# Performance work log

Hardware: AMD Instinct MI355X
Metric: run time of the kernel (lower is better)

The kernel has to match this reference:

```python
import jax, jax.numpy as jnp
import numpy as np

T_EPS = 1e-07
NUM_CAPSULE = 10
DIM_CAPSULE = 64
ROUTINGS = 5


def squash(x, axis=-1):
    # NOTE: this repo's 'squash' is just norm-division (no s/(1+s) factor)
    s = jnp.sum(x * x, axis=axis, keepdims=True)
    return x / jnp.sqrt(s + T_EPS)


def setup_inputs() -> dict:
    key = jax.random.key(0)
    k1, k2 = jax.random.split(key)
    B, N, D = 128, 512, 300
    M = NUM_CAPSULE * DIM_CAPSULE  # 640
    x = jax.random.normal(k1, (B, N, D), dtype=jnp.float32)
    # xavier_normal for shape (1, D, M): std = sqrt(2/(fan_in+fan_out))
    std = float(np.sqrt(2.0 / (D + M)))
    W = jax.random.normal(k2, (1, D, M), dtype=jnp.float32) * std
    return {"x": x, "W": W}


def reference(x, W):
    B, N, D = x.shape
    # u_hat_vecs: [B, num_capsule(i), input_num_capsule(j), dim_capsule(k)]
    u = jnp.einsum('bnd,dm->bnm', x, W[0])
    u = u.reshape(B, N, NUM_CAPSULE, DIM_CAPSULE).transpose(0, 2, 1, 3)
    b = jnp.zeros((B, NUM_CAPSULE, N), dtype=x.dtype)
    outputs = None
    for i in range(ROUTINGS):
        # softmax over the num_capsule axis (axis=1 of b), matching the
        # permute(0,2,1) -> softmax(dim=2) -> permute back in torch
        c = jax.nn.softmax(b, axis=1)
        outputs = squash(jnp.einsum('bij,bijk->bik', c, u))  # [B, num, dim]
        if i < ROUTINGS - 1:
            b = jnp.einsum('bik,bijk->bij', outputs, u)
    return outputs
```

## Files before the change

### kernel.cpp

```cpp
#include <hip/hip_runtime.h>
#include <hip/hip_bf16.h>
#include <stdint.h>

#define BQ 128
#define NJ 512
#define DD 300
#define NC 10
#define DC 64
#define MM 640
#define KP 320
#define RT 5

typedef __attribute__((ext_vector_type(8))) short short8;
typedef __attribute__((ext_vector_type(4))) float f32x4;


__global__ void k_cast_x(const float* __restrict__ x, __hip_bfloat16* __restrict__ xb) {
    int g = blockIdx.x * 256 + threadIdx.x;
    int row = g / 40, cg2 = g - row * 40;
    const float* src = x + (size_t)row * DD + cg2 * 8;
    float4 a = make_float4(0.f, 0.f, 0.f, 0.f), b4 = a;
    if (cg2 < 37) { a = *(const float4*)src; b4 = *(const float4*)(src + 4); }
    else if (cg2 == 37) { a = *(const float4*)src; }
    union { ushort u[8]; uint4 v; } o;
    float f[8] = {a.x, a.y, a.z, a.w, b4.x, b4.y, b4.z, b4.w};
#pragma unroll
    for (int e = 0; e < 8; ++e) {
        __hip_bfloat16 hh = __float2bfloat16(f[e]);
        o.u[e] = *(ushort*)&hh;
    }
    *(uint4*)(xb + (size_t)row * KP + cg2 * 8) = o.v;
}

__global__ void k_cast_w(const float* __restrict__ w, __hip_bfloat16* __restrict__ wt) {
    int idx = blockIdx.x * 256 + threadIdx.x;
    int m = idx / KP, k = idx - m * KP;
    float v = (k < DD) ? w[(size_t)k * MM + m] : 0.f;
    wt[idx] = __float2bfloat16(v);
}

__global__ void k_zero(float4* __restrict__ p) {
    p[blockIdx.x * 256 + threadIdx.x] = make_float4(0.f, 0.f, 0.f, 0.f);
}


__global__ __launch_bounds__(256)
void k_gemm(const __hip_bfloat16* __restrict__ A,
            const __hip_bfloat16* __restrict__ Bt,
            __hip_bfloat16* __restrict__ C,
            float* __restrict__ su) {
    __shared__ __align__(16) __hip_bfloat16 As[128 * 64];
    __shared__ __align__(16) __hip_bfloat16 Bs[128 * 64];

    const int L  = blockIdx.x;
    const int n0 = ((L >> 3) % 5) * 128;
    const int m0 = ((L / 40) * 8 + (L & 7)) * 128;
    const int t  = threadIdx.x;
    const int w  = t >> 6, lane = t & 63;
    const int wrow = (w >> 1) * 64, wcol = (w & 1) * 64;
    const int quad = lane >> 4, r = lane & 15;

    f32x4 acc[4][4] = {};

    const int srow = t >> 3;
    const int sl   = (t & 7) ^ (srow & 7);
    const __hip_bfloat16* ag = A  + (size_t)(m0 + srow) * KP + sl * 8;
    const __hip_bfloat16* bg = Bt + (size_t)(n0 + srow) * KP + sl * 8;

    for (int kt = 0; kt < KP / 64; ++kt) {
        __syncthreads();
#pragma unroll
        for (int s = 0; s < 4; ++s) {
            __builtin_amdgcn_global_load_lds(
                (const __attribute__((address_space(1))) void*)(ag + (size_t)s * 32 * KP + kt * 64),
                (__attribute__((address_space(3))) void*)(&As[s * 2048 + t * 8]), 16, 0, 0);
            __builtin_amdgcn_global_load_lds(
                (const __attribute__((address_space(1))) void*)(bg + (size_t)s * 32 * KP + kt * 64),
                (__attribute__((address_space(3))) void*)(&Bs[s * 2048 + t * 8]), 16, 0, 0);
        }
        __syncthreads();

#pragma unroll
        for (int hh = 0; hh < 2; ++hh) {
            short8 af[4], bf[4];
#pragma unroll
            for (int mi = 0; mi < 4; ++mi) {
                int rho = wrow + mi * 16 + r;
                int p = (hh * 4 + quad) ^ (rho & 7);
                af[mi] = *(const short8*)&As[rho * 64 + p * 8];
            }
#pragma unroll
            for (int ni = 0; ni < 4; ++ni) {
                int rho = wcol + ni * 16 + r;
                int p = (hh * 4 + quad) ^ (rho & 7);
                bf[ni] = *(const short8*)&Bs[rho * 64 + p * 8];
            }
#pragma unroll
            for (int mi = 0; mi < 4; ++mi)
#pragma unroll
                for (int ni = 0; ni < 4; ++ni)
                    acc[mi][ni] = __builtin_amdgcn_mfma_f32_16x16x32_bf16(
                        af[mi], bf[ni], acc[mi][ni], 0, 0, 0);
        }
    }

#pragma unroll
    for (int mi = 0; mi < 4; ++mi)
#pragma unroll
        for (int ni = 0; ni < 4; ++ni) {
            int col = n0 + wcol + ni * 16 + r;
#pragma unroll
            for (int p = 0; p < 4; ++p) {
                int row = m0 + wrow + mi * 16 + quad * 4 + p;
                C[(size_t)row * MM + col] = __float2bfloat16(acc[mi][ni][p]);
            }
        }

    float cs[4];
#pragma unroll
    for (int ni = 0; ni < 4; ++ni) {
        float s = 0.f;
#pragma unroll
        for (int mi = 0; mi < 4; ++mi)
#pragma unroll
            for (int p = 0; p < 4; ++p) s += acc[mi][ni][p];
        s += __shfl_xor(s, 16, 64);
        s += __shfl_xor(s, 32, 64);
        cs[ni] = s;
    }
    if (quad == 0) {
        int bb = m0 >> 9;
#pragma unroll
        for (int ni = 0; ni < 4; ++ni)
            atomicAdd(&su[(size_t)bb * MM + n0 + wcol + ni * 16 + r], cs[ni]);
    }
}


#define TJ 16
#define NT 8
#define TILE_BYTES (TJ * MM * 2)

__global__ __launch_bounds__(512)
void k_pass(const __hip_bfloat16* __restrict__ u, const float* __restrict__ pprev,
            float* __restrict__ pnext, int first) {
    __shared__ __align__(16) char smem[TILE_BYTES + 32 * 161 * 4 + 160 * 4 + MM * 4];
    ushort* ub    = (ushort*)smem;
    float*  red   = (float*)(smem + TILE_BYTES);
    float*  blj   = (float*)(smem + TILE_BYTES + 20608);
    float*  outl  = (float*)(smem + TILE_BYTES + 20608 + 640);
    float*  pored = (float*)smem;

    const int t   = threadIdx.x;
    const int blk = blockIdx.x;
    const int b   = blk >> 2, q = blk & 3;
    const int w   = t >> 6, lane = t & 63;
    const int jd  = t >> 5, kg = t & 31;

    const char* ubase = (const char*)(u + (size_t)(b * NJ + q * 128) * MM);

    uint4 sa = *(const uint4*)(ubase + t * 16);
    uint4 sb = *(const uint4*)(ubase + 8192 + t * 16);
    uint2 sc = *(const uint2*)(ubase + 16384 + t * 8);

    if (w < 5) {
        float s0, s1;
        if (first) {
            s0 = 0.1f * pprev[(size_t)b * MM + w * 64 + lane];
            s1 = 0.1f * pprev[(size_t)b * MM + 320 + w * 64 + lane];
        } else {
            const float* pp = pprev + (size_t)b * 4 * MM;
            s0 = 0.f; s1 = 0.f;
#pragma unroll
            for (int qq = 0; qq < 4; ++qq) {
                s0 += pp[qq * MM + w * 64 + lane];
                s1 += pp[qq * MM + 320 + w * 64 + lane];
            }
        }
        float q0 = s0 * s0, q1 = s1 * s1;
#pragma unroll
        for (int m = 32; m >= 1; m >>= 1) {
            q0 += __shfl_xor(q0, m, 64);
            q1 += __shfl_xor(q1, m, 64);
        }
        outl[w * 64 + lane]       = s0 * rsqrtf(q0 + 1e-7f);
        outl[320 + w * 64 + lane] = s1 * rsqrtf(q1 + 1e-7f);
    }

    float po[20];
#pragma unroll
    for (int e = 0; e < 20; ++e) po[e] = 0.f;

    for (int tt = 0; tt < NT; ++tt) {
        uint4 na, nb; uint2 nc2;
        if (tt + 1 < NT) {
            const char* ns = ubase + (size_t)(tt + 1) * TILE_BYTES;
            na  = *(const uint4*)(ns + t * 16);
            nb  = *(const uint4*)(ns + 8192 + t * 16);
            nc2 = *(const uint2*)(ns + 16384 + t * 8);
        }
        __syncthreads();
        *(uint4*)((char*)ub + t * 16)        = sa;
        *(uint4*)((char*)ub + 8192 + t * 16) = sb;
        *(uint2*)((char*)ub + 16384 + t * 8) = sc;
        __syncthreads();

        const ushort* urow = ub + jd * MM;
        uint uv[10];
#pragma unroll
        for (int i = 0; i < 10; ++i)
            uv[i] = *(const uint*)(urow + i * 64 + kg * 2);

#pragma unroll
        for (int i = 0; i < 10; ++i) {
            float u0 = __uint_as_float(uv[i] << 16);
            float u1 = __uint_as_float(uv[i] & 0xffff0000u);
            float2 oo = *(const float2*)(outl + i * 64 + kg * 2);
            red[kg * 161 + jd * 10 + i] = u0 * oo.x + u1 * oo.y;
        }
        __syncthreads();
        if (t < 160) {
            float s = 0.f;
#pragma unroll
            for (int g = 0; g < 32; ++g) s += red[g * 161 + t];
            blj[t] = s;
        }
        __syncthreads();
        float c[10];
        {
            float bl[10], mx = -1e30f;
#pragma unroll
            for (int i = 0; i < 10; ++i) { bl[i] = blj[jd * 10 + i]; mx = fmaxf(mx, bl[i]); }
            float ssum = 0.f;
#pragma unroll
            for (int i = 0; i < 10; ++i) { bl[i] = __expf(bl[i] - mx); ssum += bl[i]; }
            float inv = 1.f / ssum;
#pragma unroll
            for (int i = 0; i < 10; ++i) c[i] = bl[i] * inv;
        }
#pragma unroll
        for (int i = 0; i < 10; ++i) {
            float u0 = __uint_as_float(uv[i] << 16);
            float u1 = __uint_as_float(uv[i] & 0xffff0000u);
            po[i * 2 + 0] += c[i] * u0;
            po[i * 2 + 1] += c[i] * u1;
        }
        sa = na; sb = nb; sc = nc2;
    }

#pragma unroll
    for (int e = 0; e < 20; ++e) po[e] += __shfl_xor(po[e], 32, 64);
    __syncthreads();
    if ((t & 63) < 32) {
#pragma unroll
        for (int e = 0; e < 20; ++e) pored[(w * 32 + kg) * 20 + e] = po[e];
    }
    __syncthreads();
    for (int m = t; m < MM; m += 512) {
        int i = m >> 6, k = m & 63, kg2 = k >> 1, kd = k & 1;
        float s = 0.f;
#pragma unroll
        for (int ww = 0; ww < 8; ++ww) s += pored[(ww * 32 + kg2) * 20 + i * 2 + kd];
        pnext[(size_t)blk * MM + m] = s;
    }
}

__global__ __launch_bounds__(640)
void k_squash(const float* __restrict__ pbuf, float* __restrict__ dst) {
    int b = blockIdx.x, t = threadIdx.x;
    float s = 0.f;
#pragma unroll
    for (int qq = 0; qq < 4; ++qq) s += pbuf[(size_t)(b * 4 + qq) * MM + t];
    float sq = s * s;
#pragma unroll
    for (int m = 32; m >= 1; m >>= 1) sq += __shfl_xor(sq, m, 64);
    dst[(size_t)b * MM + t] = s * rsqrtf(sq + 1e-7f);
}


extern "C" void kernel_launch(void* const* d_in, const int* in_sizes, int n_in,
                              void* d_out, int out_size, void* d_ws, size_t ws_size,
                              hipStream_t stream) {
    const float* x = (const float*)d_in[0];
    const float* W = (const float*)d_in[1];
    float* out = (float*)d_out;

    char* ws = (char*)d_ws;
    size_t o = 0;
    __hip_bfloat16* xb = (__hip_bfloat16*)(ws + o); o += (size_t)BQ * NJ * KP * 2;
    __hip_bfloat16* wt = (__hip_bfloat16*)(ws + o); o += (size_t)MM * KP * 2;
    __hip_bfloat16* u  = (__hip_bfloat16*)(ws + o); o += (size_t)BQ * NJ * MM * 2;
    float* pb0 = (float*)(ws + o); o += (size_t)512 * MM * 4;
    float* pb1 = (float*)(ws + o); o += (size_t)512 * MM * 4;
    float* su  = (float*)(ws + o); o += (size_t)BQ * MM * 4;

    k_cast_x<<<(BQ * NJ * 40) / 256, 256, 0, stream>>>(x, xb);
    k_cast_w<<<(MM * KP) / 256, 256, 0, stream>>>(W, wt);
    k_zero<<<(BQ * MM) / (4 * 256), 256, 0, stream>>>((float4*)su);
    k_gemm<<<2560, 256, 0, stream>>>(xb, wt, u, su);

    k_pass<<<512, 512, 0, stream>>>(u, su,  pb0, 1);
    k_pass<<<512, 512, 0, stream>>>(u, pb0, pb1, 0);
    k_pass<<<512, 512, 0, stream>>>(u, pb1, pb0, 0);
    k_pass<<<512, 512, 0, stream>>>(u, pb0, pb1, 0);
    k_squash<<<BQ, 640, 0, stream>>>(pb1, out);
}
```

Before: 235.0 us.

## Replace GEMM atomics with partial-sum stores and widen routing tiles

The GEMM no longer zeroes a buffer and atomically adds column sums; each 64-row warp slab writes its partial sum to its own slot, and the first routing pass sums 8 partials. That removes the zero kernel and the atomic contention. The routing pass now processes 32 rows per tile in 4 iterations, with each thread handling 4 dims (uint2 loads), the squashed output kept as bf16 in LDS, and an occupancy hint of 2 blocks. This cuts reduction overhead and syncs per row, but raises register pressure (40 accumulators) and rounds the routing vector to bf16.

```diff
diff --git a/kernel.cpp b/kernel.cpp
--- a/kernel.cpp
+++ b/kernel.cpp
@@ -13,6 +13,9 @@
 
 typedef __attribute__((ext_vector_type(8))) short short8;
 typedef __attribute__((ext_vector_type(4))) float f32x4;
+
+__device__ inline float lo16(uint v) { return __uint_as_float(v << 16); }
+__device__ inline float hi16(uint v) { return __uint_as_float(v & 0xffff0000u); }
 
 
 __global__ void k_cast_x(const float* __restrict__ x, __hip_bfloat16* __restrict__ xb) {
@@ -39,16 +42,12 @@
     wt[idx] = __float2bfloat16(v);
 }
 
-__global__ void k_zero(float4* __restrict__ p) {
-    p[blockIdx.x * 256 + threadIdx.x] = make_float4(0.f, 0.f, 0.f, 0.f);
-}
-
 
 __global__ __launch_bounds__(256)
 void k_gemm(const __hip_bfloat16* __restrict__ A,
             const __hip_bfloat16* __restrict__ Bt,
             __hip_bfloat16* __restrict__ C,
-            float* __restrict__ su) {
+            float* __restrict__ psu) {
     __shared__ __align__(16) __hip_bfloat16 As[128 * 64];
     __shared__ __align__(16) __hip_bfloat16 Bs[128 * 64];
 
@@ -129,101 +128,99 @@
         cs[ni] = s;
     }
     if (quad == 0) {
-        int bb = m0 >> 9;
+        int mb2 = (m0 >> 6) + (wrow >> 6);
 #pragma unroll
         for (int ni = 0; ni < 4; ++ni)
-            atomicAdd(&su[(size_t)bb * MM + n0 + wcol + ni * 16 + r], cs[ni]);
-    }
-}
-
-
-#define TJ 16
-#define NT 8
+            psu[(size_t)mb2 * MM + n0 + wcol + ni * 16 + r] = cs[ni];
+    }
+}
+
+
+#define TJ 32
+#define NT 4
 #define TILE_BYTES (TJ * MM * 2)
 
-__global__ __launch_bounds__(512)
+__global__ __launch_bounds__(512, 2)
 void k_pass(const __hip_bfloat16* __restrict__ u, const float* __restrict__ pprev,
-            float* __restrict__ pnext, int first) {
-    __shared__ __align__(16) char smem[TILE_BYTES + 32 * 161 * 4 + 160 * 4 + MM * 4];
+            float* __restrict__ pnext, int nch) {
+    __shared__ __align__(16) char smem[TILE_BYTES + 16 * 321 * 4 + 320 * 4 + MM * 2];
     ushort* ub    = (ushort*)smem;
     float*  red   = (float*)(smem + TILE_BYTES);
-    float*  blj   = (float*)(smem + TILE_BYTES + 20608);
-    float*  outl  = (float*)(smem + TILE_BYTES + 20608 + 640);
+    float*  blj   = (float*)(smem + TILE_BYTES + 20544);
+    ushort* outl  = (ushort*)(smem + TILE_BYTES + 20544 + 1280);
     float*  pored = (float*)smem;
 
     const int t   = threadIdx.x;
     const int blk = blockIdx.x;
     const int b   = blk >> 2, q = blk & 3;
     const int w   = t >> 6, lane = t & 63;
-    const int jd  = t >> 5, kg = t & 31;
+    const int jd  = t >> 4, kg = t & 15;
 
     const char* ubase = (const char*)(u + (size_t)(b * NJ + q * 128) * MM);
 
-    uint4 sa = *(const uint4*)(ubase + t * 16);
-    uint4 sb = *(const uint4*)(ubase + 8192 + t * 16);
-    uint2 sc = *(const uint2*)(ubase + 16384 + t * 8);
+    uint4 s0 = *(const uint4*)(ubase + 0 * 8192 + t * 16);
+    uint4 s1 = *(const uint4*)(ubase + 1 * 8192 + t * 16);
+    uint4 s2 = *(const uint4*)(ubase + 2 * 8192 + t * 16);
+    uint4 s3 = *(const uint4*)(ubase + 3 * 8192 + t * 16);
+    uint4 s4 = *(const uint4*)(ubase + 4 * 8192 + t * 16);
 
     if (w < 5) {
-        float s0, s1;
-        if (first) {
-            s0 = 0.1f * pprev[(size_t)b * MM + w * 64 + lane];
-            s1 = 0.1f * pprev[(size_t)b * MM + 320 + w * 64 + lane];
-        } else {
-            const float* pp = pprev + (size_t)b * 4 * MM;
-            s0 = 0.f; s1 = 0.f;
-#pragma unroll
-            for (int qq = 0; qq < 4; ++qq) {
-                s0 += pp[qq * MM + w * 64 + lane];
-                s1 += pp[qq * MM + 320 + w * 64 + lane];
-            }
-        }
-        float q0 = s0 * s0, q1 = s1 * s1;
+        int i0 = w * 64 + lane, i1 = 320 + i0;
+        float a0 = 0.f, a1 = 0.f;
+        for (int qq = 0; qq < nch; ++qq) {
+            a0 += pprev[(size_t)(b * nch + qq) * MM + i0];
+            a1 += pprev[(size_t)(b * nch + qq) * MM + i1];
+        }
+        float q0 = a0 * a0, q1 = a1 * a1;
 #pragma unroll
         for (int m = 32; m >= 1; m >>= 1) {
             q0 += __shfl_xor(q0, m, 64);
             q1 += __shfl_xor(q1, m, 64);
         }
-        outl[w * 64 + lane]       = s0 * rsqrtf(q0 + 1e-7f);
-        outl[320 + w * 64 + lane] = s1 * rsqrtf(q1 + 1e-7f);
-    }
-
-    float po[20];
-#pragma unroll
-    for (int e = 0; e < 20; ++e) po[e] = 0.f;
+        __hip_bfloat16 h0 = __float2bfloat16(a0 * rsqrtf(q0 + 1e-7f));
+        __hip_bfloat16 h1 = __float2bfloat16(a1 * rsqrtf(q1 + 1e-7f));
+        outl[i0] = *(ushort*)&h0;
+        outl[i1] = *(ushort*)&h1;
+    }
+
+    float po[40];
+#pragma unroll
+    for (int e = 0; e < 40; ++e) po[e] = 0.f;
 
     for (int tt = 0; tt < NT; ++tt) {
-        uint4 na, nb; uint2 nc2;
+        uint4 n0v, n1v, n2v, n3v, n4v;
         if (tt + 1 < NT) {
             const char* ns = ubase + (size_t)(tt + 1) * TILE_BYTES;
-            na  = *(const uint4*)(ns + t * 16);
-            nb  = *(const uint4*)(ns + 8192 + t * 16);
-            nc2 = *(const uint2*)(ns + 16384 + t * 8);
-        }
-        __syncthreads();
-        *(uint4*)((char*)ub + t * 16)        = sa;
-        *(uint4*)((char*)ub + 8192 + t * 16) = sb;
-        *(uint2*)((char*)ub + 16384 + t * 8) = sc;
+            n0v = *(const uint4*)(ns + 0 * 8192 + t * 16);
+            n1v = *(const uint4*)(ns + 1 * 8192 + t * 16);
+            n2v = *(const uint4*)(ns + 2 * 8192 + t * 16);
+            n3v = *(const uint4*)(ns + 3 * 8192 + t * 16);
+            n4v = *(const uint4*)(ns + 4 * 8192 + t * 16);
+        }
+        __syncthreads();
+        *(uint4*)((char*)ub + 0 * 8192 + t * 16) = s0;
+        *(uint4*)((char*)ub + 1 * 8192 + t * 16) = s1;
+        *(uint4*)((char*)ub + 2 * 8192 + t * 16) = s2;
+        *(uint4*)((char*)ub + 3 * 8192 + t * 16) = s3;
+        *(uint4*)((char*)ub + 4 * 8192 + t * 16) = s4;
         __syncthreads();
 
         const ushort* urow = ub + jd * MM;
-        uint uv[10];
-#pragma unroll
-        for (int i = 0; i < 10; ++i)
-            uv[i] = *(const uint*)(urow + i * 64 + kg * 2);
-
+        uint2 uv[10];
 #pragma unroll
         for (int i = 0; i < 10; ++i) {
-            float u0 = __uint_as_float(uv[i] << 16);
-            float u1 = __uint_as_float(uv[i] & 0xffff0000u);
-            float2 oo = *(const float2*)(outl + i * 64 + kg * 2);
-            red[kg * 161 + jd * 10 + i] = u0 * oo.x + u1 * oo.y;
-        }
-        __syncthreads();
-        if (t < 160) {
-            float s = 0.f;
-#pragma unroll
-            for (int g = 0; g < 32; ++g) s += red[g * 161 + t];
-            blj[t] = s;
+            uv[i] = *(const uint2*)(urow + i * 64 + kg * 4);
+            uint2 ov = *(const uint2*)(outl + i * 64 + kg * 4);
+            float pb = lo16(uv[i].x) * lo16(ov.x) + hi16(uv[i].x) * hi16(ov.x)
+                     + lo16(uv[i].y) * lo16(ov.y) + hi16(uv[i].y) * hi16(ov.y);
+            red[kg * 321 + jd * 10 + i] = pb;
+        }
+        __syncthreads();
+        if (t < 320) {
+            float ss = 0.f;
+#pragma unroll
+            for (int g = 0; g < 16; ++g) ss += red[g * 321 + t];
+            blj[t] = ss;
         }
         __syncthreads();
         float c[10];
@@ -240,28 +237,33 @@
         }
 #pragma unroll
         for (int i = 0; i < 10; ++i) {
-            float u0 = __uint_as_float(uv[i] << 16);
-            float u1 = __uint_as_float(uv[i] & 0xffff0000u);
-            po[i * 2 + 0] += c[i] * u0;
-            po[i * 2 + 1] += c[i] * u1;
-        }
-        sa = na; sb = nb; sc = nc2;
-    }
-
-#pragma unroll
-    for (int e = 0; e < 20; ++e) po[e] += __shfl_xor(po[e], 32, 64);
+            po[i * 4 + 0] += c[i] * lo16(uv[i].x);
+            po[i * 4 + 1] += c[i] * hi16(uv[i].x);
+            po[i * 4 + 2] += c[i] * lo16(uv[i].y);
+            po[i * 4 + 3] += c[i] * hi16(uv[i].y);
+        }
+        s0 = n0v; s1 = n1v; s2 = n2v; s3 = n3v; s4 = n4v;
+    }
+
+#pragma unroll
+    for (int e = 0; e < 40; ++e) {
+        po[e] += __shfl_xor(po[e], 16, 64);
+        po[e] += __shfl_xor(po[e], 32, 64);
+    }
     __syncthreads();
-    if ((t & 63) < 32) {
-#pragma unroll
-        for (int e = 0; e < 20; ++e) pored[(w * 32 + kg) * 20 + e] = po[e];
+    if ((lane >> 4) == 0) {
+#pragma unroll
+        for (int i = 0; i < 10; ++i) {
+            f32x4 v = {po[i * 4 + 0], po[i * 4 + 1], po[i * 4 + 2], po[i * 4 + 3]};
+            *(f32x4*)&pored[w * 648 + i * 64 + kg * 4] = v;
+        }
     }
     __syncthreads();
     for (int m = t; m < MM; m += 512) {
-        int i = m >> 6, k = m & 63, kg2 = k >> 1, kd = k & 1;
-        float s = 0.f;
-#pragma unroll
-        for (int ww = 0; ww < 8; ++ww) s += pored[(ww * 32 + kg2) * 20 + i * 2 + kd];
-        pnext[(size_t)blk * MM + m] = s;
+        float ss = 0.f;
+#pragma unroll
+        for (int ww = 0; ww < 8; ++ww) ss += pored[ww * 648 + m];
+        pnext[(size_t)blk * MM + m] = ss;
     }
 }
 
@@ -292,16 +294,15 @@
     __hip_bfloat16* u  = (__hip_bfloat16*)(ws + o); o += (size_t)BQ * NJ * MM * 2;
     float* pb0 = (float*)(ws + o); o += (size_t)512 * MM * 4;
     float* pb1 = (float*)(ws + o); o += (size_t)512 * MM * 4;
-    float* su  = (float*)(ws + o); o += (size_t)BQ * MM * 4;
+    float* psu = (float*)(ws + o); o += (size_t)1024 * MM * 4;
 
     k_cast_x<<<(BQ * NJ * 40) / 256, 256, 0, stream>>>(x, xb);
     k_cast_w<<<(MM * KP) / 256, 256, 0, stream>>>(W, wt);
-    k_zero<<<(BQ * MM) / (4 * 256), 256, 0, stream>>>((float4*)su);
-    k_gemm<<<2560, 256, 0, stream>>>(xb, wt, u, su);
-
-    k_pass<<<512, 512, 0, stream>>>(u, su,  pb0, 1);
-    k_pass<<<512, 512, 0, stream>>>(u, pb0, pb1, 0);
-    k_pass<<<512, 512, 0, stream>>>(u, pb1, pb0, 0);
-    k_pass<<<512, 512, 0, stream>>>(u, pb0, pb1, 0);
+    k_gemm<<<2560, 256, 0, stream>>>(xb, wt, u, psu);
+
+    k_pass<<<512, 512, 0, stream>>>(u, psu, pb0, 8);
+    k_pass<<<512, 512, 0, stream>>>(u, pb0, pb1, 4);
+    k_pass<<<512, 512, 0, stream>>>(u, pb1, pb0, 4);
+    k_pass<<<512, 512, 0, stream>>>(u, pb0, pb1, 4);
     k_squash<<<BQ, 640, 0, stream>>>(pb1, out);
 }
```

Measured after the change: 269.0 us. 14.5% more time.
